# Kernel optimization log

Measured on AMD Instinct MI355X. Metric: run time of the kernel, lower is better.

The kernel has to match this reference:

```python
import jax, jax.numpy as jnp
import numpy as np

HIDDEN = 96
N_NODES = 50000
N_EDGES = 800000
IN_DIM = 256


def setup_inputs() -> dict:
    key = jax.random.key(0)
    ks = jax.random.split(key, 8)
    x = jax.random.normal(ks[0], (N_NODES, IN_DIM), dtype=jnp.float32)
    d = jax.random.uniform(ks[1], (N_NODES,), dtype=jnp.float32)
    src = jax.random.randint(ks[2], (N_EDGES,), 0, N_NODES, dtype=jnp.int32)
    dst = jax.random.randint(ks[3], (N_EDGES,), 0, N_NODES, dtype=jnp.int32)
    # Xavier-normal-ish init scaled like the torch module (gain 1.414)
    W_in = jax.random.normal(ks[4], (HIDDEN, IN_DIM), dtype=jnp.float32) * (1.414 * np.sqrt(2.0 / (HIDDEN + IN_DIM)))
    b_in = jnp.zeros((HIDDEN,), dtype=jnp.float32)
    W_gate = jax.random.normal(ks[5], (HIDDEN, 2 * HIDDEN), dtype=jnp.float32) * (1.414 * np.sqrt(2.0 / (3 * HIDDEN)))
    b_gate = jnp.zeros((HIDDEN,), dtype=jnp.float32)
    W_clf = jax.random.normal(ks[6], (2, HIDDEN), dtype=jnp.float32) * np.sqrt(2.0 / (2 + HIDDEN))
    b_clf = jnp.zeros((2,), dtype=jnp.float32)
    return {"x": x, "d": d, "src": src, "dst": dst,
            "W_in": W_in, "b_in": b_in, "W_gate": W_gate, "b_gate": b_gate,
            "W_clf": W_clf, "b_clf": b_clf}


def reference(x, d, src, dst, W_in, b_in, W_gate, b_gate, W_clf, b_clf):
    # h = input_gate(x)
    h = x @ W_in.T + b_in                                  # [N, H]
    # NOTE: the original loop reassigns the same h every iteration, so every
    # num_layer iteration produces identical (z, a); one pass is the exact math.
    h_src = h[src]                                         # [E, H] gather
    h_dst = h[dst]                                         # [E, H] gather
    h2 = jnp.concatenate([h_dst, h_src], axis=1)           # [E, 2H]
    a = jnp.tanh((h2 @ W_gate.T + b_gate) / np.sqrt(2.0 * HIDDEN))  # [E, H]
    e = d[dst] * d[src]                                    # [E]
    msg = h_src * a * e[:, None]                           # [E, H]
    z = jax.ops.segment_sum(msg, dst, num_segments=N_NODES)  # scatter-sum to dst
    z = jax.nn.log_softmax(z @ W_clf.T + b_clf, axis=-1)   # [N, 2]
    return (z, a)
```

## Files before the change

### kernel.cpp

```cpp
#include <hip/hip_runtime.h>
#include <math.h>

#define HIDDEN 96
#define NNODES 50000
#define NEDGES 800000
#define INDIM  256
#define RS 0.07216878364870323f

typedef float f32x4 __attribute__((ext_vector_type(4)));

__device__ __forceinline__ float fast_tanh(float x) {
    float e = __builtin_amdgcn_exp2f(fabsf(x) * 2.8853900817779268f);
    float t = 1.0f - 2.0f * __builtin_amdgcn_rcpf(1.0f + e);
    return copysignf(t, x);
}

__global__ void repack_kernel(const float* __restrict__ Wg, const float* __restrict__ bg,
                              float* __restrict__ V, float* __restrict__ bias2) {
    int idx = blockIdx.x * 256 + threadIdx.x;
    if (idx < 192 * 96) {
        int j = idx / 96, k = idx % 96;
        float v = (j < 96) ? Wg[j * 192 + k] : Wg[(j - 96) * 192 + 96 + k];
        V[idx] = v * RS;
    }
    if (idx < 192) bias2[idx] = (idx < 96) ? bg[idx] * RS : 0.0f;
}

__global__ __launch_bounds__(256) void gemm_nt_bias(
    const float* __restrict__ A, int lda,
    const float* __restrict__ B,
    const float* __restrict__ bias, float* __restrict__ C,
    int M, int K, int ldc) {
    __shared__ float As[128][36];
    __shared__ float Bs[96][36];
    const int tid = threadIdx.x;
    const int m0 = blockIdx.x * 128;
    const int te = tid >> 4;
    const int tc = tid & 15;
    const int ra = tid >> 3;
    const int ka = (tid & 7) * 4;

    float acc[8][6];
#pragma unroll
    for (int i = 0; i < 8; i++)
#pragma unroll
        for (int j = 0; j < 6; j++) acc[i][j] = 0.0f;

    for (int k0 = 0; k0 < K; k0 += 32) {
#pragma unroll
        for (int r = 0; r < 4; r++) {
            int row = m0 + ra + r * 32;
            float4 v = make_float4(0, 0, 0, 0);
            if (row < M) v = *(const float4*)&A[(size_t)row * lda + k0 + ka];
            *(float4*)&As[ra + r * 32][ka] = v;
        }
#pragma unroll
        for (int r = 0; r < 3; r++) {
            int row = ra + r * 32;
            float4 v = *(const float4*)&B[(size_t)row * K + k0 + ka];
            *(float4*)&Bs[row][ka] = v;
        }
        __syncthreads();
#pragma unroll
        for (int k4 = 0; k4 < 32; k4 += 4) {
            float4 af[8], bf[6];
#pragma unroll
            for (int i = 0; i < 8; i++) af[i] = *(float4*)&As[8 * te + i][k4];
#pragma unroll
            for (int j = 0; j < 6; j++) bf[j] = *(float4*)&Bs[6 * tc + j][k4];
#pragma unroll
            for (int i = 0; i < 8; i++)
#pragma unroll
                for (int j = 0; j < 6; j++)
                    acc[i][j] += af[i].x * bf[j].x + af[i].y * bf[j].y +
                                 af[i].z * bf[j].z + af[i].w * bf[j].w;
        }
        __syncthreads();
    }
#pragma unroll
    for (int i = 0; i < 8; i++) {
        int row = m0 + 8 * te + i;
        if (row < M) {
#pragma unroll
            for (int j = 0; j < 6; j++) {
                int col = 6 * tc + j;
                C[(size_t)row * ldc + col] = acc[i][j] + bias[col];
            }
        }
    }
}

__global__ __launch_bounds__(256) void gemm2_dual(
    const float* __restrict__ Ah,
    const float* __restrict__ V,
    const float* __restrict__ b2,
    float* __restrict__ Dm,
    float* __restrict__ SH,
    int M) {
    __shared__ float As[128][36];
    __shared__ float Bs[96][36];
    const int tid = threadIdx.x;
    const int m0 = blockIdx.x * 128;
    const int half = blockIdx.y;
    const int n0 = half * 96;
    const int te = tid >> 4;
    const int tc = tid & 15;
    const int ra = tid >> 3;
    const int ka = (tid & 7) * 4;

    float acc[8][6];
#pragma unroll
    for (int i = 0; i < 8; i++)
#pragma unroll
        for (int j = 0; j < 6; j++) acc[i][j] = 0.0f;

    for (int k0 = 0; k0 < 96; k0 += 32) {
#pragma unroll
        for (int r = 0; r < 4; r++) {
            int row = m0 + ra + r * 32;
            float4 v = make_float4(0, 0, 0, 0);
            if (row < M) v = *(const float4*)&Ah[(size_t)row * 192 + k0 + ka];
            *(float4*)&As[ra + r * 32][ka] = v;
        }
#pragma unroll
        for (int r = 0; r < 3; r++) {
            int row = ra + r * 32;
            float4 v = *(const float4*)&V[(size_t)(n0 + row) * 96 + k0 + ka];
            *(float4*)&Bs[row][ka] = v;
        }
        __syncthreads();
#pragma unroll
        for (int k4 = 0; k4 < 32; k4 += 4) {
            float4 af[8], bf[6];
#pragma unroll
            for (int i = 0; i < 8; i++) af[i] = *(float4*)&As[8 * te + i][k4];
#pragma unroll
            for (int j = 0; j < 6; j++) bf[j] = *(float4*)&Bs[6 * tc + j][k4];
#pragma unroll
            for (int i = 0; i < 8; i++)
#pragma unroll
                for (int j = 0; j < 6; j++)
                    acc[i][j] += af[i].x * bf[j].x + af[i].y * bf[j].y +
                                 af[i].z * bf[j].z + af[i].w * bf[j].w;
        }
        __syncthreads();
    }
    float* Cp = half ? SH : Dm;
    const int ldc = half ? 192 : 96;
#pragma unroll
    for (int i = 0; i < 8; i++) {
        int row = m0 + 8 * te + i;
        if (row < M) {
#pragma unroll
            for (int j = 0; j < 6; j++) {
                int col = 6 * tc + j;
                Cp[(size_t)row * ldc + col] = acc[i][j] + b2[n0 + col];
            }
        }
    }
}

__global__ void hist_kernel(const int* __restrict__ dst, int* __restrict__ counts) {
    int i = blockIdx.x * 256 + threadIdx.x;
    if (i < NEDGES) atomicAdd(&counts[dst[i]], 1);
}

__global__ __launch_bounds__(512) void scan1_kernel(const int* __restrict__ counts,
                                                    int* __restrict__ offsets,
                                                    int* __restrict__ btot) {
    __shared__ int sh[512];
    int tid = threadIdx.x;
    int i = blockIdx.x * 512 + tid;
    int v = (i < NNODES) ? counts[i] : 0;
    sh[tid] = v;
    __syncthreads();
    for (int off = 1; off < 512; off <<= 1) {
        int tmp = 0;
        if (tid >= off) tmp = sh[tid - off];
        __syncthreads();
        if (tid >= off) sh[tid] += tmp;
        __syncthreads();
    }
    if (i < NNODES) offsets[i] = sh[tid] - v;
    if (tid == 511) btot[blockIdx.x] = sh[511];
}

__global__ __launch_bounds__(128) void scan2_kernel(int* __restrict__ btot, int nb) {
    __shared__ int sh[128];
    int tid = threadIdx.x;
    int v = (tid < nb) ? btot[tid] : 0;
    sh[tid] = v;
    __syncthreads();
    for (int off = 1; off < 128; off <<= 1) {
        int tmp = 0;
        if (tid >= off) tmp = sh[tid - off];
        __syncthreads();
        if (tid >= off) sh[tid] += tmp;
        __syncthreads();
    }
    if (tid < nb) btot[tid] = sh[tid] - v;
}

__global__ __launch_bounds__(512) void scan3_kernel(int* __restrict__ offsets,
                                                    const int* __restrict__ btot) {
    int i = blockIdx.x * 512 + threadIdx.x;
    if (i < NNODES) offsets[i] += btot[blockIdx.x];
    if (i == 0) offsets[NNODES] = NEDGES;
}

__global__ void scatter_kernel(const int* __restrict__ src, const int* __restrict__ dst,
                               const int* __restrict__ offsets, int* __restrict__ cursor,
                               int2* __restrict__ epair) {
    int e = blockIdx.x * 256 + threadIdx.x;
    if (e < NEDGES) {
        int t = dst[e];
        int pos = offsets[t] + atomicAdd(&cursor[t], 1);
        epair[pos] = make_int2(e, src[e]);
    }
}

#define GPB 32
#define TPG 24
__global__ __launch_bounds__(768) void agg_kernel(
    const float* __restrict__ Dm, const float* __restrict__ SH,
    const float* __restrict__ dvec, const int* __restrict__ offsets,
    const int2* __restrict__ epair,
    const float* __restrict__ Wc, const float* __restrict__ bc,
    float* __restrict__ a_out, float* __restrict__ z_out) {
    __shared__ float red0[GPB * TPG];
    __shared__ float red1[GPB * TPG];
    const int t = threadIdx.x;
    const int g = t / TPG;
    const int c = t % TPG;
    const int node = blockIdx.x * GPB + g;
    float s0 = 0.0f, s1 = 0.0f;
    if (node < NNODES) {
        float4 pd = *(const float4*)&Dm[(size_t)node * 96 + 4 * c];
        float dt = dvec[node];
        int start = offsets[node], end = offsets[node + 1];
        float4 z4 = make_float4(0, 0, 0, 0);
        for (int i = start; i < end; i++) {
            int2 ep = epair[i];
            const float* base = &SH[(size_t)ep.y * 192];
            float4 ps = *(const float4*)(base + 4 * c);
            float4 hs = *(const float4*)(base + 96 + 4 * c);
            float ee = dt * dvec[ep.y];
            f32x4 a4;
            a4.x = fast_tanh(pd.x + ps.x);
            a4.y = fast_tanh(pd.y + ps.y);
            a4.z = fast_tanh(pd.z + ps.z);
            a4.w = fast_tanh(pd.w + ps.w);
            __builtin_nontemporal_store(a4, (f32x4*)&a_out[(size_t)ep.x * 96 + 4 * c]);
            z4.x += hs.x * a4.x * ee;
            z4.y += hs.y * a4.y * ee;
            z4.z += hs.z * a4.z * ee;
            z4.w += hs.w * a4.w * ee;
        }
        float4 w0 = *(const float4*)&Wc[4 * c];
        float4 w1 = *(const float4*)&Wc[96 + 4 * c];
        s0 = z4.x * w0.x + z4.y * w0.y + z4.z * w0.z + z4.w * w0.w;
        s1 = z4.x * w1.x + z4.y * w1.y + z4.z * w1.z + z4.w * w1.w;
    }
    red0[t] = s0;
    red1[t] = s1;
    __syncthreads();
    if (c == 0 && node < NNODES) {
        float a0 = bc[0], a1 = bc[1];
#pragma unroll
        for (int k = 0; k < TPG; k++) { a0 += red0[t + k]; a1 += red1[t + k]; }
        float m = fmaxf(a0, a1);
        float lse = m + logf(expf(a0 - m) + expf(a1 - m));
        z_out[2 * node + 0] = a0 - lse;
        z_out[2 * node + 1] = a1 - lse;
    }
}

extern "C" void kernel_launch(void* const* d_in, const int* in_sizes, int n_in,
                              void* d_out, int out_size, void* d_ws, size_t ws_size,
                              hipStream_t stream) {
    const float* x    = (const float*)d_in[0];
    const float* dvec = (const float*)d_in[1];
    const int*   src  = (const int*)d_in[2];
    const int*   dst  = (const int*)d_in[3];
    const float* W_in = (const float*)d_in[4];
    const float* b_in = (const float*)d_in[5];
    const float* W_g  = (const float*)d_in[6];
    const float* b_g  = (const float*)d_in[7];
    const float* W_c  = (const float*)d_in[8];
    const float* b_c  = (const float*)d_in[9];

    float* z_out = (float*)d_out;
    float* a_out = (float*)d_out + 2 * NNODES;

    char* ws = (char*)d_ws;
    float* SH      = (float*)(ws);
    float* Dm      = (float*)(ws + 38400000);
    float* V       = (float*)(ws + 57600000);
    float* b2      = (float*)(ws + 57673728);
    int*   offsets = (int*)  (ws + 57674752);
    int*   counts  = (int*)  (ws + 57874816);
    int*   cursor  = (int*)  (ws + 58074880);
    int*   btot    = (int*)  (ws + 58274944);
    int2*  epair   = (int2*) (ws + 58275456);

    hipMemsetAsync(counts, 0, NNODES * sizeof(int), stream);
    hipMemsetAsync(cursor, 0, NNODES * sizeof(int), stream);

    repack_kernel<<<dim3((192 * 96 + 255) / 256), 256, 0, stream>>>(W_g, b_g, V, b2);
    gemm_nt_bias<<<dim3((NNODES + 127) / 128), 256, 0, stream>>>(
        x, INDIM, W_in, b_in, SH + 96, NNODES, INDIM, 192);
    gemm2_dual<<<dim3((NNODES + 127) / 128, 2), 256, 0, stream>>>(
        SH + 96, V, b2, Dm, SH, NNODES);

    const int NB = (NNODES + 511) / 512;
    hist_kernel<<<dim3((NEDGES + 255) / 256), 256, 0, stream>>>(dst, counts);
    scan1_kernel<<<dim3(NB), 512, 0, stream>>>(counts, offsets, btot);
    scan2_kernel<<<dim3(1), 128, 0, stream>>>(btot, NB);
    scan3_kernel<<<dim3(NB), 512, 0, stream>>>(offsets, btot);
    scatter_kernel<<<dim3((NEDGES + 255) / 256), 256, 0, stream>>>(src, dst, offsets, cursor, epair);

    agg_kernel<<<dim3((NNODES + GPB - 1) / GPB), GPB * TPG, 0, stream>>>(
        Dm, SH, dvec, offsets, epair, W_c, b_c, a_out, z_out);
}
```

Measured before the change: 767.5 us.

## Store gathered source features in fp16, fold degree scaling, prefetch next edge

The per-source gather table (gate projection plus hidden state) now lives in fp16 instead of fp32, halving the bytes each edge gathers in the aggregation kernel. The source degree factor is folded into the stored hidden state and the destination degree is applied once after the loop, which removes a per-edge dvec load. The aggregation loop software-prefetches the next edge's pair and features. The fp16 storage adds rounding error to both the gate output and the aggregated sum, and gemm1 now writes an extra fp32 copy of H for gemm2.

```diff
diff --git a/kernel.cpp b/kernel.cpp
--- a/kernel.cpp
+++ b/kernel.cpp
@@ -1,4 +1,5 @@
 #include <hip/hip_runtime.h>
+#include <hip/hip_fp16.h>
 #include <math.h>
 
 #define HIDDEN 96
@@ -26,11 +27,10 @@
     if (idx < 192) bias2[idx] = (idx < 96) ? bg[idx] * RS : 0.0f;
 }
 
-__global__ __launch_bounds__(256) void gemm_nt_bias(
-    const float* __restrict__ A, int lda,
-    const float* __restrict__ B,
-    const float* __restrict__ bias, float* __restrict__ C,
-    int M, int K, int ldc) {
+__global__ __launch_bounds__(256) void gemm1_kernel(
+    const float* __restrict__ A, const float* __restrict__ B,
+    const float* __restrict__ bias, const float* __restrict__ dvec,
+    float* __restrict__ H, __half* __restrict__ SH, int M) {
     __shared__ float As[128][36];
     __shared__ float Bs[96][36];
     const int tid = threadIdx.x;
@@ -46,18 +46,18 @@
 #pragma unroll
         for (int j = 0; j < 6; j++) acc[i][j] = 0.0f;
 
-    for (int k0 = 0; k0 < K; k0 += 32) {
+    for (int k0 = 0; k0 < INDIM; k0 += 32) {
 #pragma unroll
         for (int r = 0; r < 4; r++) {
             int row = m0 + ra + r * 32;
             float4 v = make_float4(0, 0, 0, 0);
-            if (row < M) v = *(const float4*)&A[(size_t)row * lda + k0 + ka];
+            if (row < M) v = *(const float4*)&A[(size_t)row * INDIM + k0 + ka];
             *(float4*)&As[ra + r * 32][ka] = v;
         }
 #pragma unroll
         for (int r = 0; r < 3; r++) {
             int row = ra + r * 32;
-            float4 v = *(const float4*)&B[(size_t)row * K + k0 + ka];
+            float4 v = *(const float4*)&B[(size_t)row * INDIM + k0 + ka];
             *(float4*)&Bs[row][ka] = v;
         }
         __syncthreads();
@@ -81,22 +81,28 @@
     for (int i = 0; i < 8; i++) {
         int row = m0 + 8 * te + i;
         if (row < M) {
+            float dv = dvec[row];
+            float v[6];
 #pragma unroll
             for (int j = 0; j < 6; j++) {
                 int col = 6 * tc + j;
-                C[(size_t)row * ldc + col] = acc[i][j] + bias[col];
+                v[j] = acc[i][j] + bias[col];
+                H[(size_t)row * 96 + col] = v[j];
             }
+            __half* shp = SH + (size_t)row * 192 + 96 + 6 * tc;
+#pragma unroll
+            for (int j = 0; j < 3; j++) {
+                __half2 hv = __floats2half2_rn(v[2 * j] * dv, v[2 * j + 1] * dv);
+                *(__half2*)(shp + 2 * j) = hv;
+            }
         }
     }
 }
 
 __global__ __launch_bounds__(256) void gemm2_dual(
-    const float* __restrict__ Ah,
-    const float* __restrict__ V,
+    const float* __restrict__ H, const float* __restrict__ V,
     const float* __restrict__ b2,
-    float* __restrict__ Dm,
-    float* __restrict__ SH,
-    int M) {
+    float* __restrict__ Dm, __half* __restrict__ SH, int M) {
     __shared__ float As[128][36];
     __shared__ float Bs[96][36];
     const int tid = threadIdx.x;
@@ -119,7 +125,7 @@
         for (int r = 0; r < 4; r++) {
             int row = m0 + ra + r * 32;
             float4 v = make_float4(0, 0, 0, 0);
-            if (row < M) v = *(const float4*)&Ah[(size_t)row * 192 + k0 + ka];
+            if (row < M) v = *(const float4*)&H[(size_t)row * 96 + k0 + ka];
             *(float4*)&As[ra + r * 32][ka] = v;
         }
 #pragma unroll
@@ -145,16 +151,23 @@
         }
         __syncthreads();
     }
-    float* Cp = half ? SH : Dm;
-    const int ldc = half ? 192 : 96;
 #pragma unroll
     for (int i = 0; i < 8; i++) {
         int row = m0 + 8 * te + i;
         if (row < M) {
-#pragma unroll
-            for (int j = 0; j < 6; j++) {
-                int col = 6 * tc + j;
-                Cp[(size_t)row * ldc + col] = acc[i][j] + b2[n0 + col];
+            if (half == 0) {
+#pragma unroll
+                for (int j = 0; j < 6; j++) {
+                    int col = 6 * tc + j;
+                    Dm[(size_t)row * 96 + col] = acc[i][j] + b2[col];
+                }
+            } else {
+                __half* shp = SH + (size_t)row * 192 + 6 * tc;
+#pragma unroll
+                for (int j = 0; j < 3; j++) {
+                    __half2 hv = __floats2half2_rn(acc[i][2 * j], acc[i][2 * j + 1]);
+                    *(__half2*)(shp + 2 * j) = hv;
+                }
             }
         }
     }
@@ -222,7 +235,7 @@
 #define GPB 32
 #define TPG 24
 __global__ __launch_bounds__(768) void agg_kernel(
-    const float* __restrict__ Dm, const float* __restrict__ SH,
+    const float* __restrict__ Dm, const __half* __restrict__ SH,
     const float* __restrict__ dvec, const int* __restrict__ offsets,
     const int2* __restrict__ epair,
     const float* __restrict__ Wc, const float* __restrict__ bc,
@@ -239,23 +252,41 @@
         float dt = dvec[node];
         int start = offsets[node], end = offsets[node + 1];
         float4 z4 = make_float4(0, 0, 0, 0);
+
+        int2 ep;
+        uint2 psb, hzb;
+        if (start < end) {
+            ep = epair[start];
+            const __half* b = SH + (size_t)ep.y * 192;
+            psb = *(const uint2*)(b + 4 * c);
+            hzb = *(const uint2*)(b + 96 + 4 * c);
+        }
         for (int i = start; i < end; i++) {
-            int2 ep = epair[i];
-            const float* base = &SH[(size_t)ep.y * 192];
-            float4 ps = *(const float4*)(base + 4 * c);
-            float4 hs = *(const float4*)(base + 96 + 4 * c);
-            float ee = dt * dvec[ep.y];
+            int2 epn;
+            uint2 psn, hzn;
+            if (i + 1 < end) {
+                epn = epair[i + 1];
+                const __half* b = SH + (size_t)epn.y * 192;
+                psn = *(const uint2*)(b + 4 * c);
+                hzn = *(const uint2*)(b + 96 + 4 * c);
+            }
+            float2 p0 = __half22float2(*(const __half2*)&psb.x);
+            float2 p1 = __half22float2(*(const __half2*)&psb.y);
+            float2 h0 = __half22float2(*(const __half2*)&hzb.x);
+            float2 h1 = __half22float2(*(const __half2*)&hzb.y);
             f32x4 a4;
-            a4.x = fast_tanh(pd.x + ps.x);
-            a4.y = fast_tanh(pd.y + ps.y);
-            a4.z = fast_tanh(pd.z + ps.z);
-            a4.w = fast_tanh(pd.w + ps.w);
+            a4.x = fast_tanh(pd.x + p0.x);
+            a4.y = fast_tanh(pd.y + p0.y);
+            a4.z = fast_tanh(pd.z + p1.x);
+            a4.w = fast_tanh(pd.w + p1.y);
             __builtin_nontemporal_store(a4, (f32x4*)&a_out[(size_t)ep.x * 96 + 4 * c]);
-            z4.x += hs.x * a4.x * ee;
-            z4.y += hs.y * a4.y * ee;
-            z4.z += hs.z * a4.z * ee;
-            z4.w += hs.w * a4.w * ee;
-        }
+            z4.x += h0.x * a4.x;
+            z4.y += h0.y * a4.y;
+            z4.z += h1.x * a4.z;
+            z4.w += h1.y * a4.w;
+            ep = epn; psb = psn; hzb = hzn;
+        }
+        z4.x *= dt; z4.y *= dt; z4.z *= dt; z4.w *= dt;
         float4 w0 = *(const float4*)&Wc[4 * c];
         float4 w1 = *(const float4*)&Wc[96 + 4 * c];
         s0 = z4.x * w0.x + z4.y * w0.y + z4.z * w0.z + z4.w * w0.w;
@@ -293,24 +324,25 @@
     float* a_out = (float*)d_out + 2 * NNODES;
 
     char* ws = (char*)d_ws;
-    float* SH      = (float*)(ws);
-    float* Dm      = (float*)(ws + 38400000);
-    float* V       = (float*)(ws + 57600000);
-    float* b2      = (float*)(ws + 57673728);
-    int*   offsets = (int*)  (ws + 57674752);
-    int*   counts  = (int*)  (ws + 57874816);
-    int*   cursor  = (int*)  (ws + 58074880);
-    int*   btot    = (int*)  (ws + 58274944);
-    int2*  epair   = (int2*) (ws + 58275456);
+    __half* SH     = (__half*)(ws);
+    float*  H      = (float*) (ws + 19200000);
+    float*  Dm     = (float*) (ws + 38400000);
+    float*  V      = (float*) (ws + 57600000);
+    float*  b2     = (float*) (ws + 57673728);
+    int*    offsets= (int*)   (ws + 57674752);
+    int*    counts = (int*)   (ws + 57874816);
+    int*    cursor = (int*)   (ws + 58074880);
+    int*    btot   = (int*)   (ws + 58274944);
+    int2*   epair  = (int2*)  (ws + 58275456);
 
     hipMemsetAsync(counts, 0, NNODES * sizeof(int), stream);
     hipMemsetAsync(cursor, 0, NNODES * sizeof(int), stream);
 
     repack_kernel<<<dim3((192 * 96 + 255) / 256), 256, 0, stream>>>(W_g, b_g, V, b2);
-    gemm_nt_bias<<<dim3((NNODES + 127) / 128), 256, 0, stream>>>(
-        x, INDIM, W_in, b_in, SH + 96, NNODES, INDIM, 192);
+    gemm1_kernel<<<dim3((NNODES + 127) / 128), 256, 0, stream>>>(
+        x, W_in, b_in, dvec, H, SH, NNODES);
     gemm2_dual<<<dim3((NNODES + 127) / 128, 2), 256, 0, stream>>>(
-        SH + 96, V, b2, Dm, SH, NNODES);
+        H, V, b2, Dm, SH, NNODES);
 
     const int NB = (NNODES + 511) / 512;
     hist_kernel<<<dim3((NEDGES + 255) / 256), 256, 0, stream>>>(dst, counts);
```

Measured after the change: 806.1 us. +5.0%, slower.
